# Performance work log

Hardware: AMD Instinct MI355X
Metric: run time of the kernel (lower is better)

The kernel has to match this reference:

```python
import jax, jax.numpy as jnp
import numpy as np

D = 256; NH = 8; HD = D // NH; NL = 4; NP = 4; DFF = 1024; NLAYERS = 6; BS = 2
SHAPES = np.array([[100, 100], [50, 50], [25, 25], [13, 13]], dtype=np.int64)  # (H, W) per level
S = int((SHAPES[:, 0] * SHAPES[:, 1]).sum())  # 13294 flattened tokens


def setup_inputs() -> dict:
    key = jax.random.key(0)
    ks = jax.random.split(key, 12)
    p = lambda k, sh, sc: jax.random.normal(k, sh, jnp.float32) * sc
    return {
        "src": p(ks[0], (BS, S, D), 1.0),
        "pos": p(ks[1], (BS, S, D), 0.1),
        "valid_ratios": 0.5 + 0.5 * jax.random.uniform(ks[2], (BS, NL, 2), jnp.float32),
        "W_off": p(ks[3], (NLAYERS, D, NH * NL * NP * 2), 0.01),
        "b_off": jnp.zeros((NLAYERS, NH * NL * NP * 2), jnp.float32),
        "W_attn": p(ks[4], (NLAYERS, D, NH * NL * NP), 0.02),
        "b_attn": jnp.zeros((NLAYERS, NH * NL * NP), jnp.float32),
        "W_val": p(ks[5], (NLAYERS, D, D), 0.02),
        "b_val": jnp.zeros((NLAYERS, D), jnp.float32),
        "W_out": p(ks[6], (NLAYERS, D, D), 0.02),
        "b_out": jnp.zeros((NLAYERS, D), jnp.float32),
        "g1": jnp.ones((NLAYERS, D), jnp.float32),
        "be1": jnp.zeros((NLAYERS, D), jnp.float32),
        "W_ff1": p(ks[7], (NLAYERS, D, DFF), 0.02),
        "b_ff1": jnp.zeros((NLAYERS, DFF), jnp.float32),
        "W_ff2": p(ks[8], (NLAYERS, DFF, D), 0.02),
        "b_ff2": jnp.zeros((NLAYERS, D), jnp.float32),
        "g2": jnp.ones((NLAYERS, D), jnp.float32),
        "be2": jnp.zeros((NLAYERS, D), jnp.float32),
    }


def layer_norm(x, g, b, eps=1e-5):
    m = x.mean(-1, keepdims=True)
    v = jnp.var(x, axis=-1, keepdims=True)
    return (x - m) * jax.lax.rsqrt(v + eps) * g + b


def get_reference_points(valid_ratios):
    """Faithful port of DeformableTransformerEncoder.get_reference_points."""
    refs = []
    for lvl in range(NL):
        Hh, Ww = int(SHAPES[lvl, 0]), int(SHAPES[lvl, 1])
        ry, rx = jnp.meshgrid(jnp.linspace(0.5, Hh - 0.5, Hh, dtype=jnp.float32),
                              jnp.linspace(0.5, Ww - 0.5, Ww, dtype=jnp.float32), indexing="ij")
        ry = ry.reshape(-1)[None] / (valid_ratios[:, None, lvl, 1] * Hh)
        rx = rx.reshape(-1)[None] / (valid_ratios[:, None, lvl, 0] * Ww)
        refs.append(jnp.stack((rx, ry), -1))
    rp = jnp.concatenate(refs, 1)                       # [bs, S, 2]
    return rp[:, :, None] * valid_ratios[:, None]       # [bs, S, NL, 2]


def ms_deform_sample(value, locs, attn):
    """Multi-scale deformable attention core (grid_sample bilinear, zeros padding,
    align_corners=False).
    value: [bs,S,NH,HD]  locs: [bs,S,NH,NL,NP,2]  attn: [bs,S,NH,NL,NP]"""
    bs = value.shape[0]
    out = jnp.zeros((bs, NH, S, HD), value.dtype)
    start = 0
    for lvl in range(NL):
        Hh, Ww = int(SHAPES[lvl, 0]), int(SHAPES[lvl, 1])
        v = value[:, start:start + Hh * Ww].transpose(0, 2, 1, 3)  # [bs,NH,HW,HD]
        start += Hh * Ww
        loc = locs[:, :, :, lvl].transpose(0, 2, 1, 3, 4)           # [bs,NH,S,NP,2]
        x = loc[..., 0] * Ww - 0.5
        y = loc[..., 1] * Hh - 0.5
        x0 = jnp.floor(x)
        y0 = jnp.floor(y)
        wx1 = x - x0
        wy1 = y - y0
        acc = jnp.zeros((bs, NH, S, NP, HD), value.dtype)
        for dy in (0, 1):
            for dx in (0, 1):
                xi = x0 + dx
                yi = y0 + dy
                w = (wx1 if dx else 1.0 - wx1) * (wy1 if dy else 1.0 - wy1)
                valid = (xi >= 0) & (xi < Ww) & (yi >= 0) & (yi < Hh)
                idx = (jnp.clip(yi, 0, Hh - 1) * Ww + jnp.clip(xi, 0, Ww - 1)).astype(jnp.int32)
                g = jnp.take_along_axis(v, idx.reshape(bs, NH, S * NP, 1), axis=2)
                g = g.reshape(bs, NH, S, NP, HD)
                acc = acc + g * (w * valid)[..., None]
        out = out + (acc * attn[:, :, :, lvl].transpose(0, 2, 1, 3)[..., None]).sum(3)
    return out  # [bs,NH,S,HD]


def encoder_layer(src, ref, pos, params):
    (Wo, bo, Wa, ba, Wv, bv, Wout, bout, g1, be1, Wf1, bf1, Wf2, bf2, g2, be2) = params
    q = src + pos  # with_pos_embed
    value = (src @ Wv + bv).reshape(BS, S, NH, HD)
    off = (q @ Wo + bo).reshape(BS, S, NH, NL, NP, 2)
    attn = jax.nn.softmax((q @ Wa + ba).reshape(BS, S, NH, NL * NP), -1).reshape(BS, S, NH, NL, NP)
    # offset normalizer is (W, H) per level
    norm = jnp.asarray(np.stack([SHAPES[:, 1], SHAPES[:, 0]], -1), jnp.float32)  # [NL,2]
    locs = ref[:, :, None, :, None, :] + off / norm[None, None, None, :, None, :]
    sampled = ms_deform_sample(value, locs, attn)                    # [bs,NH,S,HD]
    src2 = sampled.transpose(0, 2, 1, 3).reshape(BS, S, D) @ Wout + bout
    src = layer_norm(src + src2, g1, be1)
    ff = jax.nn.relu(src @ Wf1 + bf1) @ Wf2 + bf2
    return layer_norm(src + ff, g2, be2)


def reference(src, pos, valid_ratios, W_off, b_off, W_attn, b_attn, W_val, b_val,
              W_out, b_out, g1, be1, W_ff1, b_ff1, W_ff2, b_ff2, g2, be2):
    ref = get_reference_points(valid_ratios)
    out = src
    for l in range(NLAYERS):
        params = (W_off[l], b_off[l], W_attn[l], b_attn[l], W_val[l], b_val[l],
                  W_out[l], b_out[l], g1[l], be1[l], W_ff1[l], b_ff1[l],
                  W_ff2[l], b_ff2[l], g2[l], be2[l])
        out = encoder_layer(out, ref, pos, params)
    return out
```

## Files before the change

kernel.cpp:

```cpp
#include <hip/hip_runtime.h>
#include <math.h>
#include <stdint.h>

#define D_MODEL 256
#define NH 8
#define HD 32
#define NL 4
#define NP 4
#define DFF 1024
#define NLAYERS 6
#define BS 2
#define S_TOK 13294
#define MTOT (BS * S_TOK)
#define MPAD 26624

typedef unsigned short u16;
typedef __attribute__((ext_vector_type(8))) __bf16 bf16x8;
typedef __attribute__((ext_vector_type(4))) float f32x4;

#define AS1 __attribute__((address_space(1)))
#define AS3 __attribute__((address_space(3)))

__device__ inline u16 bf16_rne(float f) {
    union { float f; uint32_t u; } v; v.f = f;
    uint32_t u = v.u;
    return (u16)((u + 0x7FFFu + ((u >> 16) & 1u)) >> 16);
}

#define WT_L 753664
#define WT_OA2 0
#define WT_OV 98304
#define WT_OOUT 163840
#define WT_OF1 229376
#define WT_OF2 491520

__global__ void wprep_kernel(const float* __restrict__ Wv, const float* __restrict__ Wo,
                             const float* __restrict__ Wa, const float* __restrict__ Wout,
                             const float* __restrict__ Wf1, const float* __restrict__ Wf2,
                             u16* __restrict__ dst)
{
    int idx = blockIdx.x * blockDim.x + threadIdx.x;
    if (idx >= NLAYERS * WT_L) return;
    int l = idx / WT_L;
    int r = idx - l * WT_L;
    float val;
    if (r < WT_OV) {
        int n = r >> 8, k = r & 255;
        if (n < 256) val = Wo[(size_t)l * 65536 + k * 256 + n];
        else         val = Wa[(size_t)l * 32768 + k * 128 + (n - 256)];
    } else if (r < WT_OOUT) {
        int sr = r - WT_OV; int n = sr >> 8, k = sr & 255;
        val = Wv[(size_t)l * 65536 + k * 256 + n];
    } else if (r < WT_OF1) {
        int sr = r - WT_OOUT; int n = sr >> 8, k = sr & 255;
        val = Wout[(size_t)l * 65536 + k * 256 + n];
    } else if (r < WT_OF2) {
        int sr = r - WT_OF1; int n = sr >> 8, k = sr & 255;
        val = Wf1[(size_t)l * 262144 + k * 1024 + n];
    } else {
        int sr = r - WT_OF2; int n = sr >> 10, k = sr & 1023;
        val = Wf2[(size_t)l * 262144 + k * 256 + n];
    }
    dst[(size_t)l * WT_L + r] = bf16_rne(val);
}

__global__ void refpoints_kernel(const float* __restrict__ vr, float* __restrict__ ref)
{
    int t = blockIdx.x * blockDim.x + threadIdx.x;
    if (t >= MTOT) return;
    int b = t / S_TOK;
    int s = t - b * S_TOK;
    int lvl, W, H, start;
    if (s < 10000)      { lvl = 0; W = 100; H = 100; start = 0; }
    else if (s < 12500) { lvl = 1; W = 50;  H = 50;  start = 10000; }
    else if (s < 13125) { lvl = 2; W = 25;  H = 25;  start = 12500; }
    else                { lvl = 3; W = 13;  H = 13;  start = 13125; }
    int wi = s - start;
    int y = wi / W;
    int x = wi - y * W;
    float rx = (x + 0.5f) / (vr[(b * NL + lvl) * 2 + 0] * (float)W);
    float ry = (y + 0.5f) / (vr[(b * NL + lvl) * 2 + 1] * (float)H);
#pragma unroll
    for (int l2 = 0; l2 < NL; l2++) {
        ref[((size_t)t * NL + l2) * 2 + 0] = rx * vr[(b * NL + l2) * 2 + 0];
        ref[((size_t)t * NL + l2) * 2 + 1] = ry * vr[(b * NL + l2) * 2 + 1];
    }
}

__global__ void conv0_kernel(const float* __restrict__ src, const float* __restrict__ pos,
                             u16* __restrict__ Xb, u16* __restrict__ Qb)
{
    int t = blockIdx.x * blockDim.x + threadIdx.x;
    if (t >= MTOT * 64) return;
    float4 s = ((const float4*)src)[t];
    float4 p = ((const float4*)pos)[t];
    ushort4 a, q;
    a.x = bf16_rne(s.x); a.y = bf16_rne(s.y); a.z = bf16_rne(s.z); a.w = bf16_rne(s.w);
    q.x = bf16_rne(s.x + p.x); q.y = bf16_rne(s.y + p.y);
    q.z = bf16_rne(s.z + p.z); q.w = bf16_rne(s.w + p.w);
    ((ushort4*)Xb)[t] = a;
    ((ushort4*)Qb)[t] = q;
}

template<int MODE>
__global__ __launch_bounds__(256) void gemm_bf16(
    const u16* __restrict__ Aq, const u16* __restrict__ Ax,
    const u16* __restrict__ Bt,
    const float* __restrict__ bias, const float* __restrict__ bias2,
    const float* __restrict__ bias3,
    void* __restrict__ C0, void* __restrict__ C1, void* __restrict__ C2,
    int N, int K)
{
    __shared__ __align__(16) u16 As[128 * 32];
    __shared__ __align__(16) u16 Bs[128 * 32];

    const int tid = threadIdx.x;
    const int wid = tid >> 6;
    const int lane = tid & 63;

    const int nwg = gridDim.x * gridDim.y;
    const int bid = blockIdx.y * gridDim.x + blockIdx.x;
    const int q = nwg >> 3, rr = nwg & 7;
    const int xcd = bid & 7, cidx = bid >> 3;
    const int wg = (xcd < rr ? xcd * (q + 1) : rr * (q + 1) + (xcd - rr) * q) + cidx;
    const int m0 = (wg / gridDim.x) * 128;
    const int n0 = (wg % gridDim.x) * 128;
    const int wr = wid >> 1, wc = wid & 1;

    f32x4 acc[4][4] = {};

    const u16* Ause = (MODE == 4 && n0 >= 384) ? Ax : Aq;
    const u16* a0 = Ause + (size_t)(m0 + (tid >> 2)) * K + (tid & 3) * 8;
    const u16* b0 = Bt + (size_t)(n0 + (tid >> 2)) * K + (tid & 3) * 8;
    u16* asb = As + wid * 512;
    u16* bsb = Bs + wid * 512;

    const int ko = (lane >> 4) * 8;
    const int rsel = lane & 15;

    for (int k0 = 0; k0 < K; k0 += 32) {
        __builtin_amdgcn_global_load_lds((AS1 void*)(a0 + k0), (AS3 void*)(asb), 16, 0, 0);
        __builtin_amdgcn_global_load_lds((AS1 void*)(a0 + (size_t)64 * K + k0),
                                         (AS3 void*)(asb + 2048), 16, 0, 0);
        __builtin_amdgcn_global_load_lds((AS1 void*)(b0 + k0), (AS3 void*)(bsb), 16, 0, 0);
        __builtin_amdgcn_global_load_lds((AS1 void*)(b0 + (size_t)64 * K + k0),
                                         (AS3 void*)(bsb + 2048), 16, 0, 0);
        __syncthreads();

        bf16x8 af[4], bfr[4];
#pragma unroll
        for (int i = 0; i < 4; i++) {
            af[i]  = *reinterpret_cast<const bf16x8*>(&As[(wr * 64 + i * 16 + rsel) * 32 + ko]);
            bfr[i] = *reinterpret_cast<const bf16x8*>(&Bs[(wc * 64 + i * 16 + rsel) * 32 + ko]);
        }
#pragma unroll
        for (int i = 0; i < 4; i++)
#pragma unroll
            for (int j = 0; j < 4; j++)
                acc[i][j] = __builtin_amdgcn_mfma_f32_16x16x32_bf16(af[i], bfr[j], acc[i][j], 0, 0, 0);
        __syncthreads();
    }

#pragma unroll
    for (int j = 0; j < 4; j++) {
        int col = n0 + wc * 64 + j * 16 + rsel;
        float bv;
        if (MODE == 4) bv = (n0 < 256) ? bias[col] : (n0 == 256) ? bias2[col - 256] : bias3[col - 384];
        else bv = bias[col];
#pragma unroll
        for (int i = 0; i < 4; i++) {
            int rbase = m0 + wr * 64 + i * 16 + (lane >> 4) * 4;
#pragma unroll
            for (int r2 = 0; r2 < 4; r2++) {
                int gm = rbase + r2;
                float v = acc[i][j][r2] + bv;
                if (MODE == 2) {
                    v = fmaxf(v, 0.f);
                    ((u16*)C0)[(size_t)gm * N + col] = bf16_rne(v);
                } else {
                    if (n0 < 256)       ((float*)C0)[(size_t)gm * 256 + col] = v;
                    else if (n0 == 256) ((float*)C1)[(size_t)gm * 128 + col - 256] = v;
                    else                ((u16*)C2)[(size_t)gm * 256 + col - 384] = bf16_rne(v);
                }
            }
        }
    }
}

template<int LNMODE>
__global__ __launch_bounds__(256) void gemm_ln(
    const u16* __restrict__ A, const u16* __restrict__ Bt,
    const float* __restrict__ bias,
    const float* __restrict__ Xres, const float* __restrict__ g,
    const float* __restrict__ be, const float* __restrict__ pos,
    float* __restrict__ dstf, u16* __restrict__ dstb, u16* __restrict__ dstq,
    int K, int Mguard)
{
    __shared__ __align__(16) u16 As[32 * 32];
    __shared__ __align__(16) u16 Bs[256 * 32];
    __shared__ float redS[32][4], redQ[32][4], mrow[32], irow[32];

    const int tid = threadIdx.x;
    const int wc = tid >> 6;
    const int lane = tid & 63;

    const int nwg = gridDim.x;
    const int q = nwg >> 3;
    const int wg = (blockIdx.x & 7) * q + (blockIdx.x >> 3);
    const int m0 = wg * 32;

    f32x4 acc[2][4] = {};

    const u16* a0 = A + (size_t)(m0 + (tid >> 2)) * K + (tid & 3) * 8;
    const u16* b0 = Bt + (size_t)(tid >> 2) * K + (tid & 3) * 8;
    u16* bsb = Bs + wc * 512;

    const int gsel = lane >> 4;
    const int rsel = lane & 15;
    const int ko = gsel * 8;

    for (int k0 = 0; k0 < K; k0 += 32) {
        if (wc < 2)
            __builtin_amdgcn_global_load_lds((AS1 void*)(a0 + k0),
                                             (AS3 void*)(As + wc * 512), 16, 0, 0);
#pragma unroll
        for (int ii = 0; ii < 4; ii++)
            __builtin_amdgcn_global_load_lds((AS1 void*)(b0 + (size_t)ii * 64 * K + k0),
                                             (AS3 void*)(bsb + ii * 2048), 16, 0, 0);
        __syncthreads();

        bf16x8 af[2], bfr[4];
#pragma unroll
        for (int i = 0; i < 2; i++)
            af[i]  = *reinterpret_cast<const bf16x8*>(&As[(i * 16 + rsel) * 32 + ko]);
#pragma unroll
        for (int j = 0; j < 4; j++)
            bfr[j] = *reinterpret_cast<const bf16x8*>(&Bs[(wc * 64 + j * 16 + rsel) * 32 + ko]);
#pragma unroll
        for (int i = 0; i < 2; i++)
#pragma unroll
            for (int j = 0; j < 4; j++)
                acc[i][j] = __builtin_amdgcn_mfma_f32_16x16x32_bf16(af[i], bfr[j], acc[i][j], 0, 0, 0);
        __syncthreads();
    }

    float bias_j[4], g_j[4], be_j[4];
#pragma unroll
    for (int j = 0; j < 4; j++) {
        int col = wc * 64 + j * 16 + rsel;
        bias_j[j] = bias[col]; g_j[j] = g[col]; be_j[j] = be[col];
    }

#pragma unroll
    for (int i = 0; i < 2; i++)
#pragma unroll
    for (int r = 0; r < 4; r++) {
        int row = i * 16 + gsel * 4 + r;
        int grow = m0 + row;
        float s = 0.f, qq = 0.f;
#pragma unroll
        for (int j = 0; j < 4; j++) {
            int col = wc * 64 + j * 16 + rsel;
            float xr = (grow < MTOT) ? Xres[(size_t)grow * 256 + col] : 0.f;
            float v = acc[i][j][r] + bias_j[j] + xr;
            acc[i][j][r] = v;
            s += v; qq += v * v;
        }
#pragma unroll
        for (int m = 1; m <= 8; m <<= 1) {
            s += __shfl_xor(s, m, 64);
            qq += __shfl_xor(qq, m, 64);
        }
        if (rsel == 0) { redS[row][wc] = s; redQ[row][wc] = qq; }
    }
    __syncthreads();
    if (tid < 32) {
        float s  = redS[tid][0] + redS[tid][1] + redS[tid][2] + redS[tid][3];
        float qq = redQ[tid][0] + redQ[tid][1] + redQ[tid][2] + redQ[tid][3];
        float mean = s * (1.f / 256.f);
        float var  = qq * (1.f / 256.f) - mean * mean;
        mrow[tid] = mean;
        irow[tid] = rsqrtf(var + 1e-5f);
    }
    __syncthreads();

#pragma unroll
    for (int i = 0; i < 2; i++)
#pragma unroll
    for (int r = 0; r < 4; r++) {
        int row = i * 16 + gsel * 4 + r;
        int grow = m0 + row;
        if (grow >= Mguard) continue;
        float mean = mrow[row], inv = irow[row];
#pragma unroll
        for (int j = 0; j < 4; j++) {
            int col = wc * 64 + j * 16 + rsel;
            float y = (acc[i][j][r] - mean) * inv * g_j[j] + be_j[j];
            dstf[(size_t)grow * 256 + col] = y;
            dstb[(size_t)grow * 256 + col] = bf16_rne(y);
            if (LNMODE == 2) {
                float pv = (grow < MTOT) ? pos[(size_t)grow * 256 + col] : 0.f;
                dstq[(size_t)grow * 256 + col] = bf16_rne(y + pv);
            }
        }
    }
}

__global__ __launch_bounds__(256) void msdeform_kernel(
    const u16* __restrict__ value, const float* __restrict__ off,
    const float* __restrict__ logits, const float* __restrict__ ref,
    u16* __restrict__ out)
{
    const int total = MTOT * NH * 4;
    const int Q = 415, R = 4;
    int bid = blockIdx.x;
    int xcd = bid & 7, cidx = bid >> 3;
    int wg = (xcd < R ? xcd * (Q + 1) : R * (Q + 1) + (xcd - R) * Q) + cidx;
    int t = wg * 256 + (int)threadIdx.x;
    if (t >= total) return;
    int c8 = t & 3;
    int h  = (t >> 2) & 7;
    int bs = t >> 5;
    int b  = (bs >= S_TOK) ? 1 : 0;

    const int Ws[4] = {100, 50, 25, 13};
    const int Hs[4] = {100, 50, 25, 13};
    const int st[4] = {0, 10000, 12500, 13125};

    const float* offp = off    + ((size_t)bs * NH + h) * 32;
    const float* lgp  = logits + ((size_t)bs * NH + h) * 16;
    const float* refp = ref    + (size_t)bs * NL * 2;

    float lw[16];
    {
        float4 a0 = ((const float4*)lgp)[0];
        float4 a1 = ((const float4*)lgp)[1];
        float4 a2 = ((const float4*)lgp)[2];
        float4 a3 = ((const float4*)lgp)[3];
        lw[0]=a0.x; lw[1]=a0.y; lw[2]=a0.z; lw[3]=a0.w;
        lw[4]=a1.x; lw[5]=a1.y; lw[6]=a1.z; lw[7]=a1.w;
        lw[8]=a2.x; lw[9]=a2.y; lw[10]=a2.z; lw[11]=a2.w;
        lw[12]=a3.x; lw[13]=a3.y; lw[14]=a3.z; lw[15]=a3.w;
        float mx = lw[0];
#pragma unroll
        for (int i = 1; i < 16; i++) mx = fmaxf(mx, lw[i]);
        float s = 0.f;
#pragma unroll
        for (int i = 0; i < 16; i++) { lw[i] = __expf(lw[i] - mx); s += lw[i]; }
        float inv = 1.f / s;
#pragma unroll
        for (int i = 0; i < 16; i++) lw[i] *= inv;
    }

    float acc[8] = {};

#pragma unroll
    for (int l = 0; l < NL; l++) {
        const int W = Ws[l], H = Hs[l];
        const u16* vbase = value + ((size_t)b * S_TOK + st[l]) * D_MODEL + h * HD + c8 * 8;
        const float fW = (float)W, fH = (float)H;
        const float rxw = fmaf(refp[l * 2 + 0], fW, -0.5f);
        const float ryh = fmaf(refp[l * 2 + 1], fH, -0.5f);
#pragma unroll
        for (int p = 0; p < NP; p++) {
            float x = rxw + offp[l * 8 + p * 2 + 0];
            float y = ryh + offp[l * 8 + p * 2 + 1];
            float a = lw[l * 4 + p];
            float x0f = floorf(x), y0f = floorf(y);
            float wx1 = x - x0f, wy1 = y - y0f;
            float wx0 = 1.f - wx1, wy0 = 1.f - wy1;
            int ix0 = (int)x0f, iy0 = (int)y0f;
#pragma unroll
            for (int dy = 0; dy < 2; dy++) {
                int yi = iy0 + dy;
                if (yi < 0 || yi >= H) continue;
                float wy = dy ? wy1 : wy0;
#pragma unroll
                for (int dx = 0; dx < 2; dx++) {
                    int xi = ix0 + dx;
                    if (xi < 0 || xi >= W) continue;
                    float wgt = (dx ? wx1 : wx0) * wy * a;
                    uint4 gv = *(const uint4*)(vbase + (size_t)(yi * W + xi) * D_MODEL);
                    union { uint32_t q; float f; } lo, hi;
                    lo.q = gv.x << 16; hi.q = gv.x & 0xffff0000u;
                    acc[0] = fmaf(lo.f, wgt, acc[0]); acc[1] = fmaf(hi.f, wgt, acc[1]);
                    lo.q = gv.y << 16; hi.q = gv.y & 0xffff0000u;
                    acc[2] = fmaf(lo.f, wgt, acc[2]); acc[3] = fmaf(hi.f, wgt, acc[3]);
                    lo.q = gv.z << 16; hi.q = gv.z & 0xffff0000u;
                    acc[4] = fmaf(lo.f, wgt, acc[4]); acc[5] = fmaf(hi.f, wgt, acc[5]);
                    lo.q = gv.w << 16; hi.q = gv.w & 0xffff0000u;
                    acc[6] = fmaf(lo.f, wgt, acc[6]); acc[7] = fmaf(hi.f, wgt, acc[7]);
                }
            }
        }
    }
    uint4 o;
    o.x = ((uint32_t)bf16_rne(acc[1]) << 16) | bf16_rne(acc[0]);
    o.y = ((uint32_t)bf16_rne(acc[3]) << 16) | bf16_rne(acc[2]);
    o.z = ((uint32_t)bf16_rne(acc[5]) << 16) | bf16_rne(acc[4]);
    o.w = ((uint32_t)bf16_rne(acc[7]) << 16) | bf16_rne(acc[6]);
    ((uint4*)out)[((size_t)bs * NH + h) * 4 + c8] = o;
}

extern "C" void kernel_launch(void* const* d_in, const int* in_sizes, int n_in,
                              void* d_out, int out_size, void* d_ws, size_t ws_size,
                              hipStream_t stream)
{
    const float* src    = (const float*)d_in[0];
    const float* pos    = (const float*)d_in[1];
    const float* vr     = (const float*)d_in[2];
    const float* W_off  = (const float*)d_in[3];
    const float* b_off  = (const float*)d_in[4];
    const float* W_attn = (const float*)d_in[5];
    const float* b_attn = (const float*)d_in[6];
    const float* W_val  = (const float*)d_in[7];
    const float* b_val  = (const float*)d_in[8];
    const float* W_out  = (const float*)d_in[9];
    const float* b_out  = (const float*)d_in[10];
    const float* g1     = (const float*)d_in[11];
    const float* be1    = (const float*)d_in[12];
    const float* W_ff1  = (const float*)d_in[13];
    const float* b_ff1  = (const float*)d_in[14];
    const float* W_ff2  = (const float*)d_in[15];
    const float* b_ff2  = (const float*)d_in[16];
    const float* g2     = (const float*)d_in[17];
    const float* be2    = (const float*)d_in[18];
    float* out = (float*)d_out;

    uint8_t* wp = (uint8_t*)d_ws;
    auto alloc = [&](size_t bytes) { uint8_t* p = wp; wp += (bytes + 255) & ~(size_t)255; return p; };
    float* refb   = (float*)alloc((size_t)MTOT * 8 * 4);
    float* Ybuf   = (float*)alloc((size_t)MPAD * 256 * 4);
    float* Xf     = (float*)alloc((size_t)MPAD * 256 * 4);
    float* offb   = (float*)alloc((size_t)MPAD * 256 * 4);
    float* attb   = (float*)alloc((size_t)MPAD * 128 * 4);
    u16*   valb16 = (u16*)alloc((size_t)MPAD * 256 * 2);
    uint8_t* slabB = alloc((size_t)MPAD * 256 * 2);
    uint8_t* slabC = alloc((size_t)MPAD * 256 * 2);
    u16* Wt = (u16*)alloc((size_t)NLAYERS * WT_L * 2);

    u16* Xb16   = (u16*)slabB;
    u16* samb16 = (u16*)slabB;
    u16* Qb16   = (u16*)slabC;
    u16* Yb16   = (u16*)slabC;
    u16* ffb16  = (u16*)offb;

    const int GY = MPAD / 128;
    const int GLN = MPAD / 32;
    const int MSD_BLOCKS = (MTOT * NH * 4 + 255) / 256;

    wprep_kernel<<<(NLAYERS * WT_L + 255) / 256, 256, 0, stream>>>(
        W_val, W_off, W_attn, W_out, W_ff1, W_ff2, Wt);
    refpoints_kernel<<<(MTOT + 255) / 256, 256, 0, stream>>>(vr, refb);
    conv0_kernel<<<(MTOT * 64 + 255) / 256, 256, 0, stream>>>(src, pos, Xb16, Qb16);

    for (int l = 0; l < NLAYERS; l++) {
        const float* Xres = (l == 0) ? src : Xf;
        const u16* Wl = Wt + (size_t)l * WT_L;

        gemm_bf16<4><<<dim3(5, GY), 256, 0, stream>>>(
            Qb16, Xb16, Wl + WT_OA2,
            b_off + l * 256, b_attn + l * 128, b_val + l * 256,
            offb, attb, valb16, 640, 256);
        msdeform_kernel<<<MSD_BLOCKS, 256, 0, stream>>>(
            valb16, offb, attb, refb, samb16);
        gemm_ln<1><<<GLN, 256, 0, stream>>>(
            samb16, Wl + WT_OOUT, b_out + l * 256,
            Xres, g1 + l * 256, be1 + l * 256, nullptr,
            Ybuf, Yb16, nullptr, 256, MPAD);
        gemm_bf16<2><<<dim3(8, GY), 256, 0, stream>>>(
            Yb16, nullptr, Wl + WT_OF1, b_ff1 + l * DFF, nullptr, nullptr,
            ffb16, nullptr, nullptr, 1024, 256);
        float* dst = (l == NLAYERS - 1) ? out : Xf;
        int mg = (l == NLAYERS - 1) ? MTOT : MPAD;
        gemm_ln<2><<<GLN, 256, 0, stream>>>(
            ffb16, Wl + WT_OF2, b_ff2 + l * 256,
            Ybuf, g2 + l * 256, be2 + l * 256, pos,
            dst, Xb16, Qb16, 1024, mg);
    }
}
```

Before: 1.201 ms.

## Swizzle LDS layouts in GEMMs, widen LN-GEMM K-step, store pos as bf16

Applies an XOR swizzle to the LDS tile columns in both GEMM kernels so MFMA fragment reads hit different banks and avoid bank conflicts. The fused GEMM+LayerNorm kernel moves to a 64-wide K step, halving the number of barrier-separated iterations at the cost of larger shared memory. The positional embedding is converted once to bf16 so the final LN epilogue reads half the bytes. The bf16 pos adds a small rounding change to the query input.

```diff
diff --git a/kernel.cpp b/kernel.cpp
--- a/kernel.cpp
+++ b/kernel.cpp
@@ -25,6 +25,9 @@
     union { float f; uint32_t u; } v; v.f = f;
     uint32_t u = v.u;
     return (u16)((u + 0x7FFFu + ((u >> 16) & 1u)) >> 16);
+}
+__device__ inline float bf16_to_f(u16 h) {
+    union { uint32_t u; float f; } v; v.u = (uint32_t)h << 16; return v.f;
 }
 
 #define WT_L 753664
@@ -88,18 +91,20 @@
 }
 
 __global__ void conv0_kernel(const float* __restrict__ src, const float* __restrict__ pos,
-                             u16* __restrict__ Xb, u16* __restrict__ Qb)
+                             u16* __restrict__ Xb, u16* __restrict__ Qb, u16* __restrict__ Pb)
 {
     int t = blockIdx.x * blockDim.x + threadIdx.x;
     if (t >= MTOT * 64) return;
     float4 s = ((const float4*)src)[t];
     float4 p = ((const float4*)pos)[t];
-    ushort4 a, q;
+    ushort4 a, q, pb;
     a.x = bf16_rne(s.x); a.y = bf16_rne(s.y); a.z = bf16_rne(s.z); a.w = bf16_rne(s.w);
     q.x = bf16_rne(s.x + p.x); q.y = bf16_rne(s.y + p.y);
     q.z = bf16_rne(s.z + p.z); q.w = bf16_rne(s.w + p.w);
+    pb.x = bf16_rne(p.x); pb.y = bf16_rne(p.y); pb.z = bf16_rne(p.z); pb.w = bf16_rne(p.w);
     ((ushort4*)Xb)[t] = a;
     ((ushort4*)Qb)[t] = q;
+    ((ushort4*)Pb)[t] = pb;
 }
 
 template<int MODE>
@@ -129,14 +134,15 @@
 
     f32x4 acc[4][4] = {};
 
+    const int csw = ((tid & 3) ^ ((tid >> 3) & 3)) * 8;
     const u16* Ause = (MODE == 4 && n0 >= 384) ? Ax : Aq;
-    const u16* a0 = Ause + (size_t)(m0 + (tid >> 2)) * K + (tid & 3) * 8;
-    const u16* b0 = Bt + (size_t)(n0 + (tid >> 2)) * K + (tid & 3) * 8;
+    const u16* a0 = Ause + (size_t)(m0 + (tid >> 2)) * K + csw;
+    const u16* b0 = Bt + (size_t)(n0 + (tid >> 2)) * K + csw;
     u16* asb = As + wid * 512;
     u16* bsb = Bs + wid * 512;
 
-    const int ko = (lane >> 4) * 8;
     const int rsel = lane & 15;
+    const int ksw = (((lane >> 4) ^ ((rsel >> 1) & 3))) * 8;
 
     for (int k0 = 0; k0 < K; k0 += 32) {
         __builtin_amdgcn_global_load_lds((AS1 void*)(a0 + k0), (AS3 void*)(asb), 16, 0, 0);
@@ -150,8 +156,8 @@
         bf16x8 af[4], bfr[4];
 #pragma unroll
         for (int i = 0; i < 4; i++) {
-            af[i]  = *reinterpret_cast<const bf16x8*>(&As[(wr * 64 + i * 16 + rsel) * 32 + ko]);
-            bfr[i] = *reinterpret_cast<const bf16x8*>(&Bs[(wc * 64 + i * 16 + rsel) * 32 + ko]);
+            af[i]  = *reinterpret_cast<const bf16x8*>(&As[(wr * 64 + i * 16 + rsel) * 32 + ksw]);
+            bfr[i] = *reinterpret_cast<const bf16x8*>(&Bs[(wc * 64 + i * 16 + rsel) * 32 + ksw]);
         }
 #pragma unroll
         for (int i = 0; i < 4; i++)
@@ -192,16 +198,17 @@
     const u16* __restrict__ A, const u16* __restrict__ Bt,
     const float* __restrict__ bias,
     const float* __restrict__ Xres, const float* __restrict__ g,
-    const float* __restrict__ be, const float* __restrict__ pos,
+    const float* __restrict__ be, const u16* __restrict__ posb,
     float* __restrict__ dstf, u16* __restrict__ dstb, u16* __restrict__ dstq,
     int K, int Mguard)
 {
-    __shared__ __align__(16) u16 As[32 * 32];
-    __shared__ __align__(16) u16 Bs[256 * 32];
+    __shared__ __align__(16) u16 As[32 * 64];
+    __shared__ __align__(16) u16 Bs[256 * 64];
     __shared__ float redS[32][4], redQ[32][4], mrow[32], irow[32];
 
     const int tid = threadIdx.x;
-    const int wc = tid >> 6;
+    const int wid = tid >> 6;
+    const int wc = wid;
     const int lane = tid & 63;
 
     const int nwg = gridDim.x;
@@ -211,36 +218,41 @@
 
     f32x4 acc[2][4] = {};
 
-    const u16* a0 = A + (size_t)(m0 + (tid >> 2)) * K + (tid & 3) * 8;
-    const u16* b0 = Bt + (size_t)(tid >> 2) * K + (tid & 3) * 8;
-    u16* bsb = Bs + wc * 512;
+    const int csw = ((tid & 7) ^ ((tid >> 3) & 7)) * 8;
+    const u16* a0 = A + (size_t)(m0 + (tid >> 3)) * K + csw;
+    const u16* b0 = Bt + (size_t)(tid >> 3) * K + csw;
 
     const int gsel = lane >> 4;
     const int rsel = lane & 15;
-    const int ko = gsel * 8;
-
-    for (int k0 = 0; k0 < K; k0 += 32) {
-        if (wc < 2)
-            __builtin_amdgcn_global_load_lds((AS1 void*)(a0 + k0),
-                                             (AS3 void*)(As + wc * 512), 16, 0, 0);
-#pragma unroll
-        for (int ii = 0; ii < 4; ii++)
-            __builtin_amdgcn_global_load_lds((AS1 void*)(b0 + (size_t)ii * 64 * K + k0),
-                                             (AS3 void*)(bsb + ii * 2048), 16, 0, 0);
+    const int swz = rsel & 7;
+
+    for (int k0 = 0; k0 < K; k0 += 64) {
+        __builtin_amdgcn_global_load_lds((AS1 void*)(a0 + k0),
+                                         (AS3 void*)(As + wid * 512), 16, 0, 0);
+#pragma unroll
+        for (int ii = 0; ii < 8; ii++)
+            __builtin_amdgcn_global_load_lds((AS1 void*)(b0 + (size_t)ii * 32 * K + k0),
+                                             (AS3 void*)(Bs + ii * 2048 + wid * 512), 16, 0, 0);
         __syncthreads();
 
-        bf16x8 af[2], bfr[4];
-#pragma unroll
-        for (int i = 0; i < 2; i++)
-            af[i]  = *reinterpret_cast<const bf16x8*>(&As[(i * 16 + rsel) * 32 + ko]);
-#pragma unroll
-        for (int j = 0; j < 4; j++)
-            bfr[j] = *reinterpret_cast<const bf16x8*>(&Bs[(wc * 64 + j * 16 + rsel) * 32 + ko]);
-#pragma unroll
-        for (int i = 0; i < 2; i++)
+#pragma unroll
+        for (int s = 0; s < 2; s++) {
+            const int cb = s * 4;
+            bf16x8 af[2], bfr[4];
+#pragma unroll
+            for (int i = 0; i < 2; i++)
+                af[i] = *reinterpret_cast<const bf16x8*>(
+                    &As[(i * 16 + rsel) * 64 + (((cb + gsel) ^ swz) * 8)]);
 #pragma unroll
             for (int j = 0; j < 4; j++)
-                acc[i][j] = __builtin_amdgcn_mfma_f32_16x16x32_bf16(af[i], bfr[j], acc[i][j], 0, 0, 0);
+                bfr[j] = *reinterpret_cast<const bf16x8*>(
+                    &Bs[(wc * 64 + j * 16 + rsel) * 64 + (((cb + gsel) ^ swz) * 8)]);
+#pragma unroll
+            for (int i = 0; i < 2; i++)
+#pragma unroll
+                for (int j = 0; j < 4; j++)
+                    acc[i][j] = __builtin_amdgcn_mfma_f32_16x16x32_bf16(af[i], bfr[j], acc[i][j], 0, 0, 0);
+        }
         __syncthreads();
     }
 
@@ -299,7 +311,7 @@
             dstf[(size_t)grow * 256 + col] = y;
             dstb[(size_t)grow * 256 + col] = bf16_rne(y);
             if (LNMODE == 2) {
-                float pv = (grow < MTOT) ? pos[(size_t)grow * 256 + col] : 0.f;
+                float pv = (grow < MTOT) ? bf16_to_f(posb[(size_t)grow * 256 + col]) : 0.f;
                 dstq[(size_t)grow * 256 + col] = bf16_rne(y + pv);
             }
         }
@@ -437,6 +449,7 @@
     u16*   valb16 = (u16*)alloc((size_t)MPAD * 256 * 2);
     uint8_t* slabB = alloc((size_t)MPAD * 256 * 2);
     uint8_t* slabC = alloc((size_t)MPAD * 256 * 2);
+    u16*   posb16 = (u16*)alloc((size_t)MPAD * 256 * 2);
     u16* Wt = (u16*)alloc((size_t)NLAYERS * WT_L * 2);
 
     u16* Xb16   = (u16*)slabB;
@@ -452,7 +465,7 @@
     wprep_kernel<<<(NLAYERS * WT_L + 255) / 256, 256, 0, stream>>>(
         W_val, W_off, W_attn, W_out, W_ff1, W_ff2, Wt);
     refpoints_kernel<<<(MTOT + 255) / 256, 256, 0, stream>>>(vr, refb);
-    conv0_kernel<<<(MTOT * 64 + 255) / 256, 256, 0, stream>>>(src, pos, Xb16, Qb16);
+    conv0_kernel<<<(MTOT * 64 + 255) / 256, 256, 0, stream>>>(src, pos, Xb16, Qb16, posb16);
 
     for (int l = 0; l < NLAYERS; l++) {
         const float* Xres = (l == 0) ? src : Xf;
@@ -475,7 +488,7 @@
         int mg = (l == NLAYERS - 1) ? MTOT : MPAD;
         gemm_ln<2><<<GLN, 256, 0, stream>>>(
             ffb16, Wl + WT_OF2, b_ff2 + l * 256,
-            Ybuf, g2 + l * 256, be2 + l * 256, pos,
+            Ybuf, g2 + l * 256, be2 + l * 256, posb16,
             dst, Xb16, Qb16, 1024, mg);
     }
 }
```

After: 1.097 ms. -8.6%, faster.
